# Optimization experiments

Hardware: AMD Instinct MI355X
Metric: run time of the kernel (lower is better)

The kernel has to match this reference:

```python
import jax, jax.numpy as jnp
import numpy as np

N = 50000      # nodes
E = 800000     # edges (avg degree 16)
F_IN = 64      # node_features (== GENConv out, so no input projection)
H = 64         # hidden
EXP = 2 * H    # GENConv MLP expansion dim = 128
D2 = F_IN + H  # dense-block concat dim = SAGEConv in = 128
EPS_MSG = 1e-7 # GENConv message eps
BN_EPS = 1e-5


def setup_inputs() -> dict:
    key = jax.random.key(0)
    ks = jax.random.split(key, 16)
    g = lambda k, shape, fan: jax.random.normal(k, shape, jnp.float32) / np.sqrt(fan)
    return {
        "x": jax.random.normal(ks[0], (N, F_IN), jnp.float32),
        "edge_index": jax.random.randint(ks[1], (2, E), 0, N, jnp.int32),
        # GENConv MLP: Linear(64,128) -> BatchNorm(128) -> ReLU -> Linear(128,64)
        "W1": g(ks[2], (H, EXP), H), "b1": jnp.zeros((EXP,), jnp.float32),
        "gamma": jnp.ones((EXP,), jnp.float32), "beta": jnp.zeros((EXP,), jnp.float32),
        "W2": g(ks[3], (EXP, H), EXP), "b2": jnp.zeros((H,), jnp.float32),
        # SAGEConv project Linear(128,128), lin_l Linear(128,64), lin_r Linear(128,64,bias=False)
        "Wp": g(ks[4], (D2, D2), D2), "bp": jnp.zeros((D2,), jnp.float32),
        "Wl": g(ks[5], (D2, H), D2), "bl": jnp.zeros((H,), jnp.float32),
        "Wr": g(ks[6], (D2, H), D2),
        # fc Linear(64,1)
        "Wf": g(ks[7], (H, 1), H), "bf": jnp.zeros((1,), jnp.float32),
    }


def _forward(x, W1, b1, gamma, beta, W2, b2, Wp, bp, Wl, bl, Wr, Wf, bf, src, dst):
    n = x.shape[0]
    # ---- GENConv(aggr='softmax', t=1.0): msg = relu(x_j) + eps -------------
    msg = jax.nn.relu(x[src]) + EPS_MSG                       # [E, H]
    mmax = jax.ops.segment_max(msg, dst, num_segments=n)      # per-dst, per-feature max
    mmax = jax.lax.stop_gradient(jnp.where(jnp.isfinite(mmax), mmax, 0.0))
    e = jnp.exp(msg - mmax[dst])                              # t = 1.0
    denom = jax.ops.segment_sum(e, dst, num_segments=n)
    numer = jax.ops.segment_sum(e * msg, dst, num_segments=n)
    agg = numer / jnp.where(denom > 0, denom, 1.0)            # softmax aggregation
    out = agg + x                                             # residual with x_dst
    # GENConv MLP (BatchNorm in training mode: batch stats, biased var)
    h = out @ W1 + b1
    mu = h.mean(axis=0)
    var = h.var(axis=0)
    h = (h - mu) * jax.lax.rsqrt(var + BN_EPS) * gamma + beta
    h = jax.nn.relu(h) @ W2 + b2                              # [N, H]
    # ---- DeepGCNLayer block='dense': concat input ---------------------------
    x2 = jnp.concatenate([x, h], axis=-1)                     # [N, F_IN+H]
    x2 = jax.nn.sigmoid(x2)                                   # self.relu = Sigmoid()
    # ---- SAGEConv(project=True, aggr=DeepSetsAggregation()==sum) -----------
    xp = jax.nn.relu(x2 @ Wp + bp)                            # projected source feats
    aggr = jax.ops.segment_sum(xp[src], dst, num_segments=n)  # DeepSets w/o nns = sum
    out2 = aggr @ Wl + bl + x2 @ Wr                           # root uses UNprojected x2
    out2 = jax.nn.sigmoid(out2)
    logits = out2 @ Wf + bf                                   # [N, 1]
    probs = jax.nn.sigmoid(logits)                            # training branch
    return probs, logits


def reference(x, edge_index, W1, b1, gamma, beta, W2, b2, Wp, bp, Wl, bl, Wr, Wf, bf):
    src, dst = edge_index[0], edge_index[1]
    return _forward(x, W1, b1, gamma, beta, W2, b2, Wp, bp, Wl, bl, Wr, Wf, bf, src, dst)
```

## Files before the change

### kernel.cpp

```cpp
#include <hip/hip_runtime.h>

#define F_IN 64
#define HID 64
#define EXPD 128
#define D2 128
#define MAXDEG 64
#define NPART 8

typedef __attribute__((ext_vector_type(8))) short bf16x8;
typedef __attribute__((ext_vector_type(4))) float f32x4;

__device__ __forceinline__ float sigmoidf_(float x) {
    return 1.0f / (1.0f + __expf(-x));
}
__device__ __forceinline__ unsigned bf16rne_(float f) {
    unsigned u = __float_as_uint(f);
    return (u + 0x7FFFu + ((u >> 16) & 1u)) >> 16;
}
__device__ __forceinline__ float bf16tof_(unsigned u16) {
    return __uint_as_float(u16 << 16);
}

__global__ __launch_bounds__(256) void k_prep(int* __restrict__ counts,
                                              float* __restrict__ bnsums,
                                              const float* __restrict__ x,
                                              unsigned short* __restrict__ x16,
                                              const float* __restrict__ W1,
                                              const float* __restrict__ W2,
                                              const float* __restrict__ Wp,
                                              const float* __restrict__ Wl,
                                              const float* __restrict__ Wr,
                                              short* __restrict__ dst, int n) {
    int b = blockIdx.x;
    int nzero = (n + 255) >> 8;
    if (b < nzero) {
        int i = b * 256 + threadIdx.x;
        if (i < n) counts[i] = 0;
        if (b == 0) bnsums[threadIdx.x] = 0.f;
        return;
    }
    if (b < nzero + 192) {
        int e = (b - nzero) * 256 + threadIdx.x;
        const float* src;
        int K, N, base;
        if (e < 8192)       { src = W1; K = 64;  N = 128; base = 0; }
        else if (e < 16384) { src = W2; K = 128; N = 64;  base = 8192; }
        else if (e < 32768) { src = Wp; K = 128; N = 128; base = 16384; }
        else if (e < 40960) { src = Wl; K = 128; N = 64;  base = 32768; }
        else                { src = Wr; K = 128; N = 64;  base = 40960; }
        int le = e - base;
        int j = le & 7;
        int lane = (le >> 3) & 63;
        int n16 = lane & 15, q = lane >> 4;
        int rest = le >> 9;
        int KC = K / 32;
        int kc = rest % KC, nt = rest / KC;
        int k = kc * 32 + q * 8 + j;
        int col = nt * 16 + n16;
        dst[e] = (short)bf16rne_(src[(size_t)k * N + col]);
        return;
    }
    int i0 = (b - nzero - 192) * 1024 + threadIdx.x * 4;
    if (i0 < n * F_IN) {
        float4 v = *(const float4*)(x + i0);
        uint2 pk;
        pk.x = bf16rne_(v.x) | (bf16rne_(v.y) << 16);
        pk.y = bf16rne_(v.z) | (bf16rne_(v.w) << 16);
        *(uint2*)(x16 + i0) = pk;
    }
}

__global__ __launch_bounds__(256) void k_fill(const int* __restrict__ ei,
                                              int* __restrict__ counts,
                                              unsigned short* __restrict__ csr,
                                              int nE, int n) {
    int p = blockIdx.x & (NPART - 1);
    int e = (blockIdx.x >> 3) * 256 + threadIdx.x;
    if (e >= nE) return;
    int d = ei[nE + e];
    int psz = (n + NPART - 1) / NPART;
    int lo = p * psz;
    if (d < lo || d >= lo + psz) return;
    int s = ei[e];
    int slot = atomicAdd(&counts[d], 1);
    if (slot < MAXDEG) csr[(size_t)d * MAXDEG + slot] = (unsigned short)s;
}

__global__ __launch_bounds__(256) void k_gen(const float* __restrict__ x,
                                             const unsigned short* __restrict__ x16,
                                             const int* __restrict__ counts,
                                             const unsigned short* __restrict__ csr,
                                             unsigned short* __restrict__ gen16, int n) {
    const unsigned* x32 = (const unsigned*)x16;
    int wid = threadIdx.x >> 6;
    int lane = threadIdx.x & 63;
    int H = lane >> 5, f2 = lane & 31;
    int v = blockIdx.x * 4 + wid;
    if (v >= n) return;
    int deg = counts[v];
    deg = deg > MAXDEG ? MAXDEG : deg;
    int idx = 0;
    if (lane < deg) idx = (int)csr[(size_t)v * MAXDEG + lane];
    float d0 = 0.f, d1 = 0.f, n0 = 0.f, n1 = 0.f;
    int i = 0;
    for (; i + 8 <= deg; i += 8) {
        int sA = __shfl(idx, i + 0 + H, 64);
        int sB = __shfl(idx, i + 2 + H, 64);
        int sC = __shfl(idx, i + 4 + H, 64);
        int sD = __shfl(idx, i + 6 + H, 64);
        unsigned uA = x32[(size_t)sA * 32 + f2];
        unsigned uB = x32[(size_t)sB * 32 + f2];
        unsigned uC = x32[(size_t)sC * 32 + f2];
        unsigned uD = x32[(size_t)sD * 32 + f2];
#pragma unroll
        for (int t = 0; t < 4; ++t) {
            unsigned u = t == 0 ? uA : t == 1 ? uB : t == 2 ? uC : uD;
            float m0 = fmaxf(bf16tof_(u & 0xFFFF), 0.f) + 1e-7f;
            float m1 = fmaxf(bf16tof_(u >> 16), 0.f) + 1e-7f;
            float e0 = __expf(m0), e1 = __expf(m1);
            d0 += e0; d1 += e1;
            n0 = fmaf(e0, m0, n0);
            n1 = fmaf(e1, m1, n1);
        }
    }
    for (; i + 2 <= deg; i += 2) {
        int s = __shfl(idx, i + H, 64);
        unsigned u = x32[(size_t)s * 32 + f2];
        float m0 = fmaxf(bf16tof_(u & 0xFFFF), 0.f) + 1e-7f;
        float m1 = fmaxf(bf16tof_(u >> 16), 0.f) + 1e-7f;
        float e0 = __expf(m0), e1 = __expf(m1);
        d0 += e0; d1 += e1;
        n0 = fmaf(e0, m0, n0);
        n1 = fmaf(e1, m1, n1);
    }
    if (i < deg) {
        int s = __shfl(idx, i, 64);
        if (H == 0) {
            unsigned u = x32[(size_t)s * 32 + f2];
            float m0 = fmaxf(bf16tof_(u & 0xFFFF), 0.f) + 1e-7f;
            float m1 = fmaxf(bf16tof_(u >> 16), 0.f) + 1e-7f;
            float e0 = __expf(m0), e1 = __expf(m1);
            d0 += e0; d1 += e1;
            n0 = fmaf(e0, m0, n0);
            n1 = fmaf(e1, m1, n1);
        }
    }
    d0 += __shfl_xor(d0, 32, 64);
    d1 += __shfl_xor(d1, 32, 64);
    n0 += __shfl_xor(n0, 32, 64);
    n1 += __shfl_xor(n1, 32, 64);
    if (H == 0) {
        float a0 = (deg > 0) ? (n0 / d0) : 0.f;
        float a1 = (deg > 0) ? (n1 / d1) : 0.f;
        float2 xv = *(const float2*)(x + (size_t)v * F_IN + f2 * 2);
        ((unsigned*)gen16)[(size_t)v * 32 + f2] =
            bf16rne_(a0 + xv.x) | (bf16rne_(a1 + xv.y) << 16);
    }
}

__global__ __launch_bounds__(256) void k_gemm1(const unsigned short* __restrict__ gen16,
                                               const short* __restrict__ Wf,
                                               const float* __restrict__ b1,
                                               unsigned short* __restrict__ h16,
                                               float* __restrict__ bnsums, int n) {
    __shared__ short As[64 * 64];
    __shared__ float bnred[256];
    int tid = threadIdx.x;
    int rblk = blockIdx.x * 64;
    if (tid < 256) bnred[tid] = 0.f;
#pragma unroll
    for (int it = 0; it < 2; ++it) {
        int c = it * 256 + tid;
        int rr = c & 63, q8 = c >> 6;
        int gr = rblk + rr;
        gr = gr < n ? gr : n - 1;
        uint4 v = *(const uint4*)(gen16 + (size_t)gr * F_IN + q8 * 8);
        int slot = ((rr >> 4) * 2 + (q8 >> 2)) * 64 + (q8 & 3) * 16 + (rr & 15);
        *(uint4*)(As + slot * 8) = v;
    }
    __syncthreads();
    int L = tid & 63, w = tid >> 6;
    int q = L >> 4, n16 = L & 15;
    int mt_base = (w & 1) * 2;
    int nt_base = (w >> 1) * 4;
    f32x4 acc[2][4];
#pragma unroll
    for (int mt = 0; mt < 2; ++mt)
#pragma unroll
        for (int nt = 0; nt < 4; ++nt) acc[mt][nt] = (f32x4){0.f, 0.f, 0.f, 0.f};
#pragma unroll
    for (int kc = 0; kc < 2; ++kc) {
        bf16x8 a0 = *(const bf16x8*)(As + (((mt_base + 0) * 2 + kc) * 64 + L) * 8);
        bf16x8 a1 = *(const bf16x8*)(As + (((mt_base + 1) * 2 + kc) * 64 + L) * 8);
#pragma unroll
        for (int nt = 0; nt < 4; ++nt) {
            bf16x8 b = *(const bf16x8*)(Wf + (size_t)(((nt_base + nt) * 2 + kc) * 64 + L) * 8);
            acc[0][nt] = __builtin_amdgcn_mfma_f32_16x16x32_bf16(a0, b, acc[0][nt], 0, 0, 0);
            acc[1][nt] = __builtin_amdgcn_mfma_f32_16x16x32_bf16(a1, b, acc[1][nt], 0, 0, 0);
        }
    }
#pragma unroll
    for (int nt = 0; nt < 4; ++nt) {
        int col = (nt_base + nt) * 16 + n16;
        float bv = b1[col];
        float s = 0.f, s2 = 0.f;
#pragma unroll
        for (int mt = 0; mt < 2; ++mt)
#pragma unroll
            for (int r = 0; r < 4; ++r) {
                int row = rblk + (w & 1) * 32 + mt * 16 + q * 4 + r;
                float hv = acc[mt][nt][r] + bv;
                if (row < n) {
                    h16[(size_t)row * EXPD + col] = (unsigned short)bf16rne_(hv);
                    s += hv;
                    s2 = fmaf(hv, hv, s2);
                }
            }
        s += __shfl_xor(s, 16, 64);
        s += __shfl_xor(s, 32, 64);
        s2 += __shfl_xor(s2, 16, 64);
        s2 += __shfl_xor(s2, 32, 64);
        if (q == 0) {
            atomicAdd(&bnred[col], s);
            atomicAdd(&bnred[128 + col], s2);
        }
    }
    __syncthreads();
    if (tid < 256) atomicAdd(&bnsums[tid], bnred[tid]);
}

__global__ __launch_bounds__(256) void k_mlp2a(const unsigned short* __restrict__ h16,
                                               const float* __restrict__ bnsums,
                                               const float* __restrict__ gamma,
                                               const float* __restrict__ beta,
                                               const short* __restrict__ Wf,
                                               const float* __restrict__ b2,
                                               const float* __restrict__ x,
                                               unsigned short* __restrict__ x2_16,
                                               float inv_n, int n) {
    __shared__ short As[128 * 128];
    __shared__ float ssl[256];
    int tid = threadIdx.x;
    int rblk = blockIdx.x * 128;
    if (tid < 128) {
        float mu = bnsums[tid] * inv_n;
        float var = fmaf(-mu, mu, bnsums[128 + tid] * inv_n);
        float rs = rsqrtf(fmaxf(var, 0.f) + 1e-5f);
        float scale = gamma[tid] * rs;
        ssl[tid] = scale;
        ssl[128 + tid] = fmaf(-mu, scale, beta[tid]);
    }
    __syncthreads();
#pragma unroll
    for (int it = 0; it < 8; ++it) {
        int c = it * 256 + tid;
        int rr = c & 127, q8 = c >> 7;
        int gr = rblk + rr;
        gr = gr < n ? gr : n - 1;
        uint4 v = *(const uint4*)(h16 + (size_t)gr * EXPD + q8 * 8);
        float4 sc1 = *(const float4*)(ssl + q8 * 8);
        float4 sc2 = *(const float4*)(ssl + q8 * 8 + 4);
        float4 sh1 = *(const float4*)(ssl + 128 + q8 * 8);
        float4 sh2 = *(const float4*)(ssl + 128 + q8 * 8 + 4);
        float o0 = fmaxf(fmaf(bf16tof_(v.x & 0xFFFF), sc1.x, sh1.x), 0.f);
        float o1 = fmaxf(fmaf(bf16tof_(v.x >> 16),    sc1.y, sh1.y), 0.f);
        float o2 = fmaxf(fmaf(bf16tof_(v.y & 0xFFFF), sc1.z, sh1.z), 0.f);
        float o3 = fmaxf(fmaf(bf16tof_(v.y >> 16),    sc1.w, sh1.w), 0.f);
        float o4 = fmaxf(fmaf(bf16tof_(v.z & 0xFFFF), sc2.x, sh2.x), 0.f);
        float o5 = fmaxf(fmaf(bf16tof_(v.z >> 16),    sc2.y, sh2.y), 0.f);
        float o6 = fmaxf(fmaf(bf16tof_(v.w & 0xFFFF), sc2.z, sh2.z), 0.f);
        float o7 = fmaxf(fmaf(bf16tof_(v.w >> 16),    sc2.w, sh2.w), 0.f);
        uint4 pk;
        pk.x = bf16rne_(o0) | (bf16rne_(o1) << 16);
        pk.y = bf16rne_(o2) | (bf16rne_(o3) << 16);
        pk.z = bf16rne_(o4) | (bf16rne_(o5) << 16);
        pk.w = bf16rne_(o6) | (bf16rne_(o7) << 16);
        int slot = ((rr >> 4) * 4 + (q8 >> 2)) * 64 + (q8 & 3) * 16 + (rr & 15);
        *(uint4*)(As + slot * 8) = pk;
    }
    __syncthreads();
    int L = tid & 63, w = tid >> 6;
    int q = L >> 4, n16 = L & 15;
    int mt_base = w * 2;
    f32x4 acc[2][4];
#pragma unroll
    for (int mt = 0; mt < 2; ++mt)
#pragma unroll
        for (int nt = 0; nt < 4; ++nt) acc[mt][nt] = (f32x4){0.f, 0.f, 0.f, 0.f};
#pragma unroll
    for (int kc = 0; kc < 4; ++kc) {
        bf16x8 a0 = *(const bf16x8*)(As + (((mt_base + 0) * 4 + kc) * 64 + L) * 8);
        bf16x8 a1 = *(const bf16x8*)(As + (((mt_base + 1) * 4 + kc) * 64 + L) * 8);
#pragma unroll
        for (int nt = 0; nt < 4; ++nt) {
            bf16x8 b = *(const bf16x8*)(Wf + (size_t)((nt * 4 + kc) * 64 + L) * 8);
            acc[0][nt] = __builtin_amdgcn_mfma_f32_16x16x32_bf16(a0, b, acc[0][nt], 0, 0, 0);
            acc[1][nt] = __builtin_amdgcn_mfma_f32_16x16x32_bf16(a1, b, acc[1][nt], 0, 0, 0);
        }
    }
#pragma unroll
    for (int it = 0; it < 8; ++it) {
        int i = it * 256 + tid;
        int rr = i >> 4, c4 = i & 15;
        int row = rblk + rr;
        if (row < n) {
            float4 xv = *(const float4*)(x + (size_t)row * F_IN + c4 * 4);
            uint2 pk;
            pk.x = bf16rne_(sigmoidf_(xv.x)) | (bf16rne_(sigmoidf_(xv.y)) << 16);
            pk.y = bf16rne_(sigmoidf_(xv.z)) | (bf16rne_(sigmoidf_(xv.w)) << 16);
            *(uint2*)(x2_16 + (size_t)row * D2 + c4 * 4) = pk;
        }
    }
#pragma unroll
    for (int nt = 0; nt < 4; ++nt) {
        int col = nt * 16 + n16;
        float bv = b2[col];
#pragma unroll
        for (int mt = 0; mt < 2; ++mt)
#pragma unroll
            for (int r = 0; r < 4; ++r) {
                int row = rblk + w * 32 + mt * 16 + q * 4 + r;
                if (row < n)
                    x2_16[(size_t)row * D2 + 64 + col] =
                        (unsigned short)bf16rne_(sigmoidf_(acc[mt][nt][r] + bv));
            }
    }
}

__global__ __launch_bounds__(256) void k_mlp2b(const unsigned short* __restrict__ x2_16,
                                               const short* __restrict__ Wfp,
                                               const short* __restrict__ Wfl,
                                               const float* __restrict__ bp,
                                               unsigned short* __restrict__ yp16, int n) {
    __shared__ short As[64 * 128];
    int tid = threadIdx.x;
    int rblk = blockIdx.x * 64;
#pragma unroll
    for (int it = 0; it < 4; ++it) {
        int c = it * 256 + tid;
        int rr = c & 63, q8 = c >> 6;
        int gr = rblk + rr;
        gr = gr < n ? gr : n - 1;
        uint4 v = *(const uint4*)(x2_16 + (size_t)gr * D2 + q8 * 8);
        int slot = ((rr >> 4) * 4 + (q8 >> 2)) * 64 + (q8 & 3) * 16 + (rr & 15);
        *(uint4*)(As + slot * 8) = v;
    }
    __syncthreads();
    int L = tid & 63, w = tid >> 6;
    int q = L >> 4, n16 = L & 15;
    int mt_base = (w & 1) * 2;
    int nt_base = (w >> 1) * 4;
    f32x4 acc[2][4];
#pragma unroll
    for (int mt = 0; mt < 2; ++mt)
#pragma unroll
        for (int nt = 0; nt < 4; ++nt) acc[mt][nt] = (f32x4){0.f, 0.f, 0.f, 0.f};
#pragma unroll
    for (int kc = 0; kc < 4; ++kc) {
        bf16x8 a0 = *(const bf16x8*)(As + (((mt_base + 0) * 4 + kc) * 64 + L) * 8);
        bf16x8 a1 = *(const bf16x8*)(As + (((mt_base + 1) * 4 + kc) * 64 + L) * 8);
#pragma unroll
        for (int nt = 0; nt < 4; ++nt) {
            bf16x8 b = *(const bf16x8*)(Wfp + (size_t)(((nt_base + nt) * 4 + kc) * 64 + L) * 8);
            acc[0][nt] = __builtin_amdgcn_mfma_f32_16x16x32_bf16(a0, b, acc[0][nt], 0, 0, 0);
            acc[1][nt] = __builtin_amdgcn_mfma_f32_16x16x32_bf16(a1, b, acc[1][nt], 0, 0, 0);
        }
    }
    __syncthreads();
#pragma unroll
    for (int nt = 0; nt < 4; ++nt) {
        int kk = (nt_base + nt) * 16 + n16;
        float bv = bp[kk];
        int q8b = kk >> 3, jb = kk & 7;
#pragma unroll
        for (int mt = 0; mt < 2; ++mt)
#pragma unroll
            for (int r = 0; r < 4; ++r) {
                int rr2 = (w & 1) * 32 + mt * 16 + q * 4 + r;
                float xv = fmaxf(acc[mt][nt][r] + bv, 0.f);
                int slot = ((rr2 >> 4) * 4 + (q8b >> 2)) * 64 + (q8b & 3) * 16 + (rr2 & 15);
                As[slot * 8 + jb] = (short)bf16rne_(xv);
            }
    }
    __syncthreads();
    f32x4 acc2[4];
#pragma unroll
    for (int nt = 0; nt < 4; ++nt) acc2[nt] = (f32x4){0.f, 0.f, 0.f, 0.f};
#pragma unroll
    for (int kc = 0; kc < 4; ++kc) {
        bf16x8 a = *(const bf16x8*)(As + ((w * 4 + kc) * 64 + L) * 8);
#pragma unroll
        for (int nt = 0; nt < 4; ++nt) {
            bf16x8 b = *(const bf16x8*)(Wfl + (size_t)((nt * 4 + kc) * 64 + L) * 8);
            acc2[nt] = __builtin_amdgcn_mfma_f32_16x16x32_bf16(a, b, acc2[nt], 0, 0, 0);
        }
    }
#pragma unroll
    for (int nt = 0; nt < 4; ++nt) {
        int col = nt * 16 + n16;
#pragma unroll
        for (int r = 0; r < 4; ++r) {
            int row = rblk + w * 16 + q * 4 + r;
            if (row < n)
                yp16[(size_t)row * HID + col] = (unsigned short)bf16rne_(acc2[nt][r]);
        }
    }
}

__global__ __launch_bounds__(256) void k_sage(const unsigned short* __restrict__ yp16,
                                              const int* __restrict__ counts,
                                              const unsigned short* __restrict__ csr,
                                              unsigned short* __restrict__ aggr16, int n) {
    const unsigned* yp32 = (const unsigned*)yp16;
    int wid = threadIdx.x >> 6;
    int lane = threadIdx.x & 63;
    int H = lane >> 5, f2 = lane & 31;
    int v = blockIdx.x * 4 + wid;
    if (v >= n) return;
    int deg = counts[v];
    deg = deg > MAXDEG ? MAXDEG : deg;
    int idx = 0;
    if (lane < deg) idx = (int)csr[(size_t)v * MAXDEG + lane];
    float a0 = 0.f, a1 = 0.f;
    int i = 0;
    for (; i + 8 <= deg; i += 8) {
        int sA = __shfl(idx, i + 0 + H, 64);
        int sB = __shfl(idx, i + 2 + H, 64);
        int sC = __shfl(idx, i + 4 + H, 64);
        int sD = __shfl(idx, i + 6 + H, 64);
        unsigned uA = yp32[(size_t)sA * 32 + f2];
        unsigned uB = yp32[(size_t)sB * 32 + f2];
        unsigned uC = yp32[(size_t)sC * 32 + f2];
        unsigned uD = yp32[(size_t)sD * 32 + f2];
        a0 += bf16tof_(uA & 0xFFFF) + bf16tof_(uB & 0xFFFF) +
              bf16tof_(uC & 0xFFFF) + bf16tof_(uD & 0xFFFF);
        a1 += bf16tof_(uA >> 16) + bf16tof_(uB >> 16) +
              bf16tof_(uC >> 16) + bf16tof_(uD >> 16);
    }
    for (; i + 2 <= deg; i += 2) {
        int s = __shfl(idx, i + H, 64);
        unsigned u = yp32[(size_t)s * 32 + f2];
        a0 += bf16tof_(u & 0xFFFF);
        a1 += bf16tof_(u >> 16);
    }
    if (i < deg) {
        int s = __shfl(idx, i, 64);
        if (H == 0) {
            unsigned u = yp32[(size_t)s * 32 + f2];
            a0 += bf16tof_(u & 0xFFFF);
            a1 += bf16tof_(u >> 16);
        }
    }
    a0 += __shfl_xor(a0, 32, 64);
    a1 += __shfl_xor(a1, 32, 64);
    if (H == 0)
        ((unsigned*)aggr16)[(size_t)v * 32 + f2] = bf16rne_(a0) | (bf16rne_(a1) << 16);
}

__global__ __launch_bounds__(256) void k_final(const unsigned short* __restrict__ aggr16,
                                               const unsigned short* __restrict__ x2_16,
                                               const short* __restrict__ Wfr,
                                               const float* __restrict__ bl,
                                               const float* __restrict__ Wfv,
                                               const float* __restrict__ bf,
                                               float* __restrict__ out, int n) {
    __shared__ short As[128 * 128];
    int tid = threadIdx.x;
    int rblk = blockIdx.x * 128;
#pragma unroll
    for (int it = 0; it < 8; ++it) {
        int c = it * 256 + tid;
        int rr = c & 127, q8 = c >> 7;
        int gr = rblk + rr;
        gr = gr < n ? gr : n - 1;
        uint4 v = *(const uint4*)(x2_16 + (size_t)gr * D2 + q8 * 8);
        int slot = ((rr >> 4) * 4 + (q8 >> 2)) * 64 + (q8 & 3) * 16 + (rr & 15);
        *(uint4*)(As + slot * 8) = v;
    }
    __syncthreads();
    int L = tid & 63, w = tid >> 6;
    int q = L >> 4, n16 = L & 15;
    int mt_base = w * 2;
    f32x4 acc[2][4];
#pragma unroll
    for (int mt = 0; mt < 2; ++mt)
#pragma unroll
        for (int nt = 0; nt < 4; ++nt) acc[mt][nt] = (f32x4){0.f, 0.f, 0.f, 0.f};
#pragma unroll
    for (int kc = 0; kc < 4; ++kc) {
        bf16x8 a0 = *(const bf16x8*)(As + (((mt_base + 0) * 4 + kc) * 64 + L) * 8);
        bf16x8 a1 = *(const bf16x8*)(As + (((mt_base + 1) * 4 + kc) * 64 + L) * 8);
#pragma unroll
        for (int nt = 0; nt < 4; ++nt) {
            bf16x8 b = *(const bf16x8*)(Wfr + (size_t)((nt * 4 + kc) * 64 + L) * 8);
            acc[0][nt] = __builtin_amdgcn_mfma_f32_16x16x32_bf16(a0, b, acc[0][nt], 0, 0, 0);
            acc[1][nt] = __builtin_amdgcn_mfma_f32_16x16x32_bf16(a1, b, acc[1][nt], 0, 0, 0);
        }
    }
    float blv[4], wfv[4];
#pragma unroll
    for (int nt = 0; nt < 4; ++nt) {
        blv[nt] = bl[nt * 16 + n16];
        wfv[nt] = Wfv[nt * 16 + n16];
    }
    float bf0 = bf[0];
#pragma unroll
    for (int mt = 0; mt < 2; ++mt)
#pragma unroll
        for (int r = 0; r < 4; ++r) {
            int row = rblk + w * 32 + mt * 16 + q * 4 + r;
            int rowc = row < n ? row : n - 1;
            float t = 0.f;
#pragma unroll
            for (int nt = 0; nt < 4; ++nt) {
                float ag = bf16tof_(aggr16[(size_t)rowc * HID + nt * 16 + n16]);
                t = fmaf(sigmoidf_(acc[mt][nt][r] + blv[nt] + ag), wfv[nt], t);
            }
            t += __shfl_xor(t, 1, 64);
            t += __shfl_xor(t, 2, 64);
            t += __shfl_xor(t, 4, 64);
            t += __shfl_xor(t, 8, 64);
            if (n16 == 0 && row < n) {
                float lg = t + bf0;
                out[row] = sigmoidf_(lg);
                out[n + row] = lg;
            }
        }
}

extern "C" void kernel_launch(void* const* d_in, const int* in_sizes, int n_in,
                              void* d_out, int out_size, void* d_ws, size_t ws_size,
                              hipStream_t stream) {
    const float* x     = (const float*)d_in[0];
    const int*   ei    = (const int*)d_in[1];
    const float* W1    = (const float*)d_in[2];
    const float* b1    = (const float*)d_in[3];
    const float* gamma = (const float*)d_in[4];
    const float* beta  = (const float*)d_in[5];
    const float* W2    = (const float*)d_in[6];
    const float* b2    = (const float*)d_in[7];
    const float* Wp    = (const float*)d_in[8];
    const float* bp    = (const float*)d_in[9];
    const float* Wl    = (const float*)d_in[10];
    const float* bl    = (const float*)d_in[11];
    const float* Wr    = (const float*)d_in[12];
    const float* Wfv   = (const float*)d_in[13];
    const float* bf    = (const float*)d_in[14];
    const int n = in_sizes[0] / F_IN;
    const int e = in_sizes[1] / 2;

    char* ws = (char*)d_ws;
    size_t off = 0;
    auto alloc = [&](size_t bytes) -> void* {
        void* p = (void*)(ws + off);
        off += (bytes + 255) & ~(size_t)255;
        return p;
    };
    int*            counts = (int*)alloc((size_t)n * 4);
    unsigned short* csr    = (unsigned short*)alloc((size_t)n * MAXDEG * 2);
    float*          bnsums = (float*)alloc(256 * 4);
    unsigned short* x16    = (unsigned short*)alloc((size_t)n * F_IN * 2);
    unsigned short* gen16  = (unsigned short*)alloc((size_t)n * F_IN * 2);
    unsigned short* h16    = (unsigned short*)alloc((size_t)n * EXPD * 2);
    unsigned short* x2_16  = (unsigned short*)alloc((size_t)n * D2 * 2);
    unsigned short* yp16   = (unsigned short*)alloc((size_t)n * HID * 2);
    unsigned short* aggr16 = (unsigned short*)alloc((size_t)n * HID * 2);
    short*          wfrag  = (short*)alloc(49152 * 2);

    float* out = (float*)d_out;
    const int nb64  = (n + 63) / 64;
    const int nb128 = (n + 127) / 128;
    const int nb4   = (n + 3) / 4;
    const int nprep = ((n + 255) / 256) + 192 + ((n * F_IN + 1023) / 1024);

    k_prep<<<nprep, 256, 0, stream>>>(counts, bnsums, x, x16, W1, W2, Wp, Wl, Wr,
                                      wfrag, n);
    k_fill<<<((e + 255) / 256) * NPART, 256, 0, stream>>>(ei, counts, csr, e, n);
    k_gen<<<nb4, 256, 0, stream>>>(x, x16, counts, csr, gen16, n);
    k_gemm1<<<nb64, 256, 0, stream>>>(gen16, wfrag, b1, h16, bnsums, n);
    k_mlp2a<<<nb128, 256, 0, stream>>>(h16, bnsums, gamma, beta, wfrag + 8192, b2,
                                       x, x2_16, 1.0f / (float)n, n);
    k_mlp2b<<<nb64, 256, 0, stream>>>(x2_16, wfrag + 16384, wfrag + 32768, bp,
                                      yp16, n);
    k_sage<<<nb4, 256, 0, stream>>>(yp16, counts, csr, aggr16, n);
    k_final<<<nb128, 256, 0, stream>>>(aggr16, x2_16, wfrag + 40960, bl, Wfv, bf,
                                       out, n);
}
```

Baseline: 242.9 us.

## Merge CSR fill with prep, memset counters, widen gathers to 4 features per lane

Replaces the zeroing part of the prep kernel with a hipMemsetAsync over counts and bnsums, then fuses the CSR fill into the weight and x conversion kernel, removing one launch. The GENConv and SAGE gather kernels now have each lane load 8 bytes (4 bf16 features) and handle 4 edges per wave step instead of 2, cutting shuffle and loop overhead. Residual and sigmoid reads of x use the bf16 copy instead of fp32, reducing bandwidth at some precision cost in the residual and concat inputs.

Result: no change. 245.3 us (+1.0%).

```diff
diff --git a/kernel.cpp b/kernel.cpp
--- a/kernel.cpp
+++ b/kernel.cpp
@@ -21,26 +21,35 @@
     return __uint_as_float(u16 << 16);
 }
 
-__global__ __launch_bounds__(256) void k_prep(int* __restrict__ counts,
-                                              float* __restrict__ bnsums,
-                                              const float* __restrict__ x,
-                                              unsigned short* __restrict__ x16,
-                                              const float* __restrict__ W1,
-                                              const float* __restrict__ W2,
-                                              const float* __restrict__ Wp,
-                                              const float* __restrict__ Wl,
-                                              const float* __restrict__ Wr,
-                                              short* __restrict__ dst, int n) {
+__global__ __launch_bounds__(256) void k_fillprep(const int* __restrict__ ei,
+                                                  int* __restrict__ counts,
+                                                  unsigned short* __restrict__ csr,
+                                                  const float* __restrict__ x,
+                                                  unsigned short* __restrict__ x16,
+                                                  const float* __restrict__ W1,
+                                                  const float* __restrict__ W2,
+                                                  const float* __restrict__ Wp,
+                                                  const float* __restrict__ Wl,
+                                                  const float* __restrict__ Wr,
+                                                  short* __restrict__ dst,
+                                                  int nE, int n, int nfillb) {
     int b = blockIdx.x;
-    int nzero = (n + 255) >> 8;
-    if (b < nzero) {
-        int i = b * 256 + threadIdx.x;
-        if (i < n) counts[i] = 0;
-        if (b == 0) bnsums[threadIdx.x] = 0.f;
+    if (b < nfillb) {
+        int p = b & (NPART - 1);
+        int e = (b >> 3) * 256 + threadIdx.x;
+        if (e >= nE) return;
+        int d = ei[nE + e];
+        int psz = (n + NPART - 1) / NPART;
+        int lo = p * psz;
+        if (d < lo || d >= lo + psz) return;
+        int s = ei[e];
+        int slot = atomicAdd(&counts[d], 1);
+        if (slot < MAXDEG) csr[(size_t)d * MAXDEG + slot] = (unsigned short)s;
         return;
     }
-    if (b < nzero + 192) {
-        int e = (b - nzero) * 256 + threadIdx.x;
+    b -= nfillb;
+    if (b < 192) {
+        int e = b * 256 + threadIdx.x;
         const float* src;
         int K, N, base;
         if (e < 8192)       { src = W1; K = 64;  N = 128; base = 0; }
@@ -60,7 +69,7 @@
         dst[e] = (short)bf16rne_(src[(size_t)k * N + col]);
         return;
     }
-    int i0 = (b - nzero - 192) * 1024 + threadIdx.x * 4;
+    int i0 = (b - 192) * 1024 + threadIdx.x * 4;
     if (i0 < n * F_IN) {
         float4 v = *(const float4*)(x + i0);
         uint2 pk;
@@ -70,91 +79,75 @@
     }
 }
 
-__global__ __launch_bounds__(256) void k_fill(const int* __restrict__ ei,
-                                              int* __restrict__ counts,
-                                              unsigned short* __restrict__ csr,
-                                              int nE, int n) {
-    int p = blockIdx.x & (NPART - 1);
-    int e = (blockIdx.x >> 3) * 256 + threadIdx.x;
-    if (e >= nE) return;
-    int d = ei[nE + e];
-    int psz = (n + NPART - 1) / NPART;
-    int lo = p * psz;
-    if (d < lo || d >= lo + psz) return;
-    int s = ei[e];
-    int slot = atomicAdd(&counts[d], 1);
-    if (slot < MAXDEG) csr[(size_t)d * MAXDEG + slot] = (unsigned short)s;
-}
-
-__global__ __launch_bounds__(256) void k_gen(const float* __restrict__ x,
-                                             const unsigned short* __restrict__ x16,
+__global__ __launch_bounds__(256) void k_gen(const unsigned short* __restrict__ x16,
                                              const int* __restrict__ counts,
                                              const unsigned short* __restrict__ csr,
                                              unsigned short* __restrict__ gen16, int n) {
-    const unsigned* x32 = (const unsigned*)x16;
+    const uint2* x64 = (const uint2*)x16;
     int wid = threadIdx.x >> 6;
     int lane = threadIdx.x & 63;
-    int H = lane >> 5, f2 = lane & 31;
+    int Q = lane >> 4, f4 = lane & 15;
     int v = blockIdx.x * 4 + wid;
     if (v >= n) return;
     int deg = counts[v];
     deg = deg > MAXDEG ? MAXDEG : deg;
     int idx = 0;
     if (lane < deg) idx = (int)csr[(size_t)v * MAXDEG + lane];
-    float d0 = 0.f, d1 = 0.f, n0 = 0.f, n1 = 0.f;
+    float d0 = 0.f, d1 = 0.f, d2 = 0.f, d3 = 0.f;
+    float n0 = 0.f, n1 = 0.f, n2 = 0.f, n3 = 0.f;
+#define GEN_PROC(u)                                                         \
+    {                                                                       \
+        float m0 = fmaxf(bf16tof_((u).x & 0xFFFF), 0.f) + 1e-7f;            \
+        float m1 = fmaxf(bf16tof_((u).x >> 16), 0.f) + 1e-7f;               \
+        float m2 = fmaxf(bf16tof_((u).y & 0xFFFF), 0.f) + 1e-7f;            \
+        float m3 = fmaxf(bf16tof_((u).y >> 16), 0.f) + 1e-7f;               \
+        float e0 = __expf(m0), e1 = __expf(m1), e2 = __expf(m2), e3 = __expf(m3); \
+        d0 += e0; d1 += e1; d2 += e2; d3 += e3;                             \
+        n0 = fmaf(e0, m0, n0); n1 = fmaf(e1, m1, n1);                       \
+        n2 = fmaf(e2, m2, n2); n3 = fmaf(e3, m3, n3);                       \
+    }
     int i = 0;
-    for (; i + 8 <= deg; i += 8) {
-        int sA = __shfl(idx, i + 0 + H, 64);
-        int sB = __shfl(idx, i + 2 + H, 64);
-        int sC = __shfl(idx, i + 4 + H, 64);
-        int sD = __shfl(idx, i + 6 + H, 64);
-        unsigned uA = x32[(size_t)sA * 32 + f2];
-        unsigned uB = x32[(size_t)sB * 32 + f2];
-        unsigned uC = x32[(size_t)sC * 32 + f2];
-        unsigned uD = x32[(size_t)sD * 32 + f2];
-#pragma unroll
-        for (int t = 0; t < 4; ++t) {
-            unsigned u = t == 0 ? uA : t == 1 ? uB : t == 2 ? uC : uD;
-            float m0 = fmaxf(bf16tof_(u & 0xFFFF), 0.f) + 1e-7f;
-            float m1 = fmaxf(bf16tof_(u >> 16), 0.f) + 1e-7f;
-            float e0 = __expf(m0), e1 = __expf(m1);
-            d0 += e0; d1 += e1;
-            n0 = fmaf(e0, m0, n0);
-            n1 = fmaf(e1, m1, n1);
-        }
-    }
-    for (; i + 2 <= deg; i += 2) {
-        int s = __shfl(idx, i + H, 64);
-        unsigned u = x32[(size_t)s * 32 + f2];
-        float m0 = fmaxf(bf16tof_(u & 0xFFFF), 0.f) + 1e-7f;
-        float m1 = fmaxf(bf16tof_(u >> 16), 0.f) + 1e-7f;
-        float e0 = __expf(m0), e1 = __expf(m1);
-        d0 += e0; d1 += e1;
-        n0 = fmaf(e0, m0, n0);
-        n1 = fmaf(e1, m1, n1);
-    }
-    if (i < deg) {
-        int s = __shfl(idx, i, 64);
-        if (H == 0) {
-            unsigned u = x32[(size_t)s * 32 + f2];
-            float m0 = fmaxf(bf16tof_(u & 0xFFFF), 0.f) + 1e-7f;
-            float m1 = fmaxf(bf16tof_(u >> 16), 0.f) + 1e-7f;
-            float e0 = __expf(m0), e1 = __expf(m1);
-            d0 += e0; d1 += e1;
-            n0 = fmaf(e0, m0, n0);
-            n1 = fmaf(e1, m1, n1);
-        }
-    }
-    d0 += __shfl_xor(d0, 32, 64);
-    d1 += __shfl_xor(d1, 32, 64);
-    n0 += __shfl_xor(n0, 32, 64);
-    n1 += __shfl_xor(n1, 32, 64);
-    if (H == 0) {
+    for (; i + 16 <= deg; i += 16) {
+        int sA = __shfl(idx, i + Q, 64);
+        int sB = __shfl(idx, i + 4 + Q, 64);
+        int sC = __shfl(idx, i + 8 + Q, 64);
+        int sD = __shfl(idx, i + 12 + Q, 64);
+        uint2 uA = x64[(size_t)sA * 16 + f4];
+        uint2 uB = x64[(size_t)sB * 16 + f4];
+        uint2 uC = x64[(size_t)sC * 16 + f4];
+        uint2 uD = x64[(size_t)sD * 16 + f4];
+        GEN_PROC(uA); GEN_PROC(uB); GEN_PROC(uC); GEN_PROC(uD);
+    }
+    for (; i < deg; i += 4) {
+        int s = __shfl(idx, i + Q, 64);
+        if (Q < deg - i) {
+            uint2 u = x64[(size_t)s * 16 + f4];
+            GEN_PROC(u);
+        }
+    }
+#undef GEN_PROC
+    d0 += __shfl_xor(d0, 16, 64); d0 += __shfl_xor(d0, 32, 64);
+    d1 += __shfl_xor(d1, 16, 64); d1 += __shfl_xor(d1, 32, 64);
+    d2 += __shfl_xor(d2, 16, 64); d2 += __shfl_xor(d2, 32, 64);
+    d3 += __shfl_xor(d3, 16, 64); d3 += __shfl_xor(d3, 32, 64);
+    n0 += __shfl_xor(n0, 16, 64); n0 += __shfl_xor(n0, 32, 64);
+    n1 += __shfl_xor(n1, 16, 64); n1 += __shfl_xor(n1, 32, 64);
+    n2 += __shfl_xor(n2, 16, 64); n2 += __shfl_xor(n2, 32, 64);
+    n3 += __shfl_xor(n3, 16, 64); n3 += __shfl_xor(n3, 32, 64);
+    if (Q == 0) {
         float a0 = (deg > 0) ? (n0 / d0) : 0.f;
         float a1 = (deg > 0) ? (n1 / d1) : 0.f;
-        float2 xv = *(const float2*)(x + (size_t)v * F_IN + f2 * 2);
-        ((unsigned*)gen16)[(size_t)v * 32 + f2] =
-            bf16rne_(a0 + xv.x) | (bf16rne_(a1 + xv.y) << 16);
+        float a2 = (deg > 0) ? (n2 / d2) : 0.f;
+        float a3 = (deg > 0) ? (n3 / d3) : 0.f;
+        uint2 xv = x64[(size_t)v * 16 + f4];
+        float r0 = a0 + bf16tof_(xv.x & 0xFFFF);
+        float r1 = a1 + bf16tof_(xv.x >> 16);
+        float r2 = a2 + bf16tof_(xv.y & 0xFFFF);
+        float r3 = a3 + bf16tof_(xv.y >> 16);
+        uint2 o;
+        o.x = bf16rne_(r0) | (bf16rne_(r1) << 16);
+        o.y = bf16rne_(r2) | (bf16rne_(r3) << 16);
+        ((uint2*)gen16)[(size_t)v * 16 + f4] = o;
     }
 }
 
@@ -235,7 +228,7 @@
                                                const float* __restrict__ beta,
                                                const short* __restrict__ Wf,
                                                const float* __restrict__ b2,
-                                               const float* __restrict__ x,
+                                               const unsigned short* __restrict__ x16,
                                                unsigned short* __restrict__ x2_16,
                                                float inv_n, int n) {
     __shared__ short As[128 * 128];
@@ -304,10 +297,14 @@
         int rr = i >> 4, c4 = i & 15;
         int row = rblk + rr;
         if (row < n) {
-            float4 xv = *(const float4*)(x + (size_t)row * F_IN + c4 * 4);
+            uint2 xv = ((const uint2*)x16)[(size_t)row * 16 + c4];
+            float s0 = sigmoidf_(bf16tof_(xv.x & 0xFFFF));
+            float s1 = sigmoidf_(bf16tof_(xv.x >> 16));
+            float s2 = sigmoidf_(bf16tof_(xv.y & 0xFFFF));
+            float s3 = sigmoidf_(bf16tof_(xv.y >> 16));
             uint2 pk;
-            pk.x = bf16rne_(sigmoidf_(xv.x)) | (bf16rne_(sigmoidf_(xv.y)) << 16);
-            pk.y = bf16rne_(sigmoidf_(xv.z)) | (bf16rne_(sigmoidf_(xv.w)) << 16);
+            pk.x = bf16rne_(s0) | (bf16rne_(s1) << 16);
+            pk.y = bf16rne_(s2) | (bf16rne_(s3) << 16);
             *(uint2*)(x2_16 + (size_t)row * D2 + c4 * 4) = pk;
         }
     }
@@ -411,50 +408,54 @@
                                               const int* __restrict__ counts,
                                               const unsigned short* __restrict__ csr,
                                               unsigned short* __restrict__ aggr16, int n) {
-    const unsigned* yp32 = (const unsigned*)yp16;
+    const uint2* yp64 = (const uint2*)yp16;
     int wid = threadIdx.x >> 6;
     int lane = threadIdx.x & 63;
-    int H = lane >> 5, f2 = lane & 31;
+    int Q = lane >> 4, f4 = lane & 15;
     int v = blockIdx.x * 4 + wid;
     if (v >= n) return;
     int deg = counts[v];
     deg = deg > MAXDEG ? MAXDEG : deg;
     int idx = 0;
     if (lane < deg) idx = (int)csr[(size_t)v * MAXDEG + lane];
-    float a0 = 0.f, a1 = 0.f;
+    float a0 = 0.f, a1 = 0.f, a2 = 0.f, a3 = 0.f;
+#define SAGE_PROC(u)                                \
+    {                                               \
+        a0 += bf16tof_((u).x & 0xFFFF);             \
+        a1 += bf16tof_((u).x >> 16);                \
+        a2 += bf16tof_((u).y & 0xFFFF);             \
+        a3 += bf16tof_((u).y >> 16);                \
+    }
     int i = 0;
-    for (; i + 8 <= deg; i += 8) {
-        int sA = __shfl(idx, i + 0 + H, 64);
-        int sB = __shfl(idx, i + 2 + H, 64);
-        int sC = __shfl(idx, i + 4 + H, 64);
-        int sD = __shfl(idx, i + 6 + H, 64);
-        unsigned uA = yp32[(size_t)sA * 32 + f2];
-        unsigned uB = yp32[(size_t)sB * 32 + f2];
-        unsigned uC = yp32[(size_t)sC * 32 + f2];
-        unsigned uD = yp32[(size_t)sD * 32 + f2];
-        a0 += bf16tof_(uA & 0xFFFF) + bf16tof_(uB & 0xFFFF) +
-              bf16tof_(uC & 0xFFFF) + bf16tof_(uD & 0xFFFF);
-        a1 += bf16tof_(uA >> 16) + bf16tof_(uB >> 16) +
-              bf16tof_(uC >> 16) + bf16tof_(uD >> 16);
-    }
-    for (; i + 2 <= deg; i += 2) {
-        int s = __shfl(idx, i + H, 64);
-        unsigned u = yp32[(size_t)s * 32 + f2];
-        a0 += bf16tof_(u & 0xFFFF);
-        a1 += bf16tof_(u >> 16);
-    }
-    if (i < deg) {
-        int s = __shfl(idx, i, 64);
-        if (H == 0) {
-            unsigned u = yp32[(size_t)s * 32 + f2];
-            a0 += bf16tof_(u & 0xFFFF);
-            a1 += bf16tof_(u >> 16);
-        }
-    }
-    a0 += __shfl_xor(a0, 32, 64);
-    a1 += __shfl_xor(a1, 32, 64);
-    if (H == 0)
-        ((unsigned*)aggr16)[(size_t)v * 32 + f2] = bf16rne_(a0) | (bf16rne_(a1) << 16);
+    for (; i + 16 <= deg; i += 16) {
+        int sA = __shfl(idx, i + Q, 64);
+        int sB = __shfl(idx, i + 4 + Q, 64);
+        int sC = __shfl(idx, i + 8 + Q, 64);
+        int sD = __shfl(idx, i + 12 + Q, 64);
+        uint2 uA = yp64[(size_t)sA * 16 + f4];
+        uint2 uB = yp64[(size_t)sB * 16 + f4];
+        uint2 uC = yp64[(size_t)sC * 16 + f4];
+        uint2 uD = yp64[(size_t)sD * 16 + f4];
+        SAGE_PROC(uA); SAGE_PROC(uB); SAGE_PROC(uC); SAGE_PROC(uD);
+    }
+    for (; i < deg; i += 4) {
+        int s = __shfl(idx, i + Q, 64);
+        if (Q < deg - i) {
+            uint2 u = yp64[(size_t)s * 16 + f4];
+            SAGE_PROC(u);
+        }
+    }
+#undef SAGE_PROC
+    a0 += __shfl_xor(a0, 16, 64); a0 += __shfl_xor(a0, 32, 64);
+    a1 += __shfl_xor(a1, 16, 64); a1 += __shfl_xor(a1, 32, 64);
+    a2 += __shfl_xor(a2, 16, 64); a2 += __shfl_xor(a2, 32, 64);
+    a3 += __shfl_xor(a3, 16, 64); a3 += __shfl_xor(a3, 32, 64);
+    if (Q == 0) {
+        uint2 o;
+        o.x = bf16rne_(a0) | (bf16rne_(a1) << 16);
+        o.y = bf16rne_(a2) | (bf16rne_(a3) << 16);
+        ((uint2*)aggr16)[(size_t)v * 16 + f4] = o;
+    }
 }
 
 __global__ __launch_bounds__(256) void k_final(const unsigned short* __restrict__ aggr16,
@@ -557,8 +558,8 @@
         return p;
     };
     int*            counts = (int*)alloc((size_t)n * 4);
+    float*          bnsums = (float*)alloc(256 * 4);
     unsigned short* csr    = (unsigned short*)alloc((size_t)n * MAXDEG * 2);
-    float*          bnsums = (float*)alloc(256 * 4);
     unsigned short* x16    = (unsigned short*)alloc((size_t)n * F_IN * 2);
     unsigned short* gen16  = (unsigned short*)alloc((size_t)n * F_IN * 2);
     unsigned short* h16    = (unsigned short*)alloc((size_t)n * EXPD * 2);
@@ -571,15 +572,18 @@
     const int nb64  = (n + 63) / 64;
     const int nb128 = (n + 127) / 128;
     const int nb4   = (n + 3) / 4;
-    const int nprep = ((n + 255) / 256) + 192 + ((n * F_IN + 1023) / 1024);
-
-    k_prep<<<nprep, 256, 0, stream>>>(counts, bnsums, x, x16, W1, W2, Wp, Wl, Wr,
-                                      wfrag, n);
-    k_fill<<<((e + 255) / 256) * NPART, 256, 0, stream>>>(ei, counts, csr, e, n);
-    k_gen<<<nb4, 256, 0, stream>>>(x, x16, counts, csr, gen16, n);
+    const int nfillb = ((e + 255) / 256) * NPART;
+    const int nfp = nfillb + 192 + ((n * F_IN + 1023) / 1024);
+
+    size_t zlen = ((((size_t)n * 4) + 255) & ~(size_t)255) + 1024;
+    hipMemsetAsync(counts, 0, zlen, stream);
+
+    k_fillprep<<<nfp, 256, 0, stream>>>(ei, counts, csr, x, x16, W1, W2, Wp, Wl,
+                                        Wr, wfrag, e, n, nfillb);
+    k_gen<<<nb4, 256, 0, stream>>>(x16, counts, csr, gen16, n);
     k_gemm1<<<nb64, 256, 0, stream>>>(gen16, wfrag, b1, h16, bnsums, n);
     k_mlp2a<<<nb128, 256, 0, stream>>>(h16, bnsums, gamma, beta, wfrag + 8192, b2,
-                                       x, x2_16, 1.0f / (float)n, n);
+                                       x16, x2_16, 1.0f / (float)n, n);
     k_mlp2b<<<nb64, 256, 0, stream>>>(x2_16, wfrag + 16384, wfrag + 32768, bp,
                                       yp16, n);
     k_sage<<<nb4, 256, 0, stream>>>(yp16, counts, csr, aggr16, n);
```

## Fuse CSR fill into prep kernel, memset counters, read bf16 x downstream

Applied to the files above, without the earlier changes.

Zeroing of the degree counters and BN sums moves to a single hipMemsetAsync, and the CSR edge fill is merged into the prep kernel, dropping the 8-way partitioned fill pass that reread the edge list once per partition. The GEN residual and the sigmoid(x) half of x2 now read the bf16 copy of x instead of the fp32 original, halving those reads. The trade-off is that atomics are no longer grouped by destination partition, which may hurt locality. Using bf16 x in the residual and sigmoid also adds extra rounding error.

Measured after the change: 247.0 us. About the same (+1.7%).

```diff
diff --git a/kernel.cpp b/kernel.cpp
--- a/kernel.cpp
+++ b/kernel.cpp
@@ -5,7 +5,6 @@
 #define EXPD 128
 #define D2 128
 #define MAXDEG 64
-#define NPART 8
 
 typedef __attribute__((ext_vector_type(8))) short bf16x8;
 typedef __attribute__((ext_vector_type(4))) float f32x4;
@@ -21,26 +20,31 @@
     return __uint_as_float(u16 << 16);
 }
 
-__global__ __launch_bounds__(256) void k_prep(int* __restrict__ counts,
-                                              float* __restrict__ bnsums,
-                                              const float* __restrict__ x,
-                                              unsigned short* __restrict__ x16,
-                                              const float* __restrict__ W1,
-                                              const float* __restrict__ W2,
-                                              const float* __restrict__ Wp,
-                                              const float* __restrict__ Wl,
-                                              const float* __restrict__ Wr,
-                                              short* __restrict__ dst, int n) {
+__global__ __launch_bounds__(256) void k_fillprep(const int* __restrict__ ei,
+                                                  int* __restrict__ counts,
+                                                  unsigned short* __restrict__ csr,
+                                                  const float* __restrict__ x,
+                                                  unsigned short* __restrict__ x16,
+                                                  const float* __restrict__ W1,
+                                                  const float* __restrict__ W2,
+                                                  const float* __restrict__ Wp,
+                                                  const float* __restrict__ Wl,
+                                                  const float* __restrict__ Wr,
+                                                  short* __restrict__ dst,
+                                                  int nE, int n, int nfillb) {
     int b = blockIdx.x;
-    int nzero = (n + 255) >> 8;
-    if (b < nzero) {
-        int i = b * 256 + threadIdx.x;
-        if (i < n) counts[i] = 0;
-        if (b == 0) bnsums[threadIdx.x] = 0.f;
+    if (b < nfillb) {
+        int e = b * 256 + threadIdx.x;
+        if (e >= nE) return;
+        int s = ei[e];
+        int d = ei[nE + e];
+        int slot = atomicAdd(&counts[d], 1);
+        if (slot < MAXDEG) csr[(size_t)d * MAXDEG + slot] = (unsigned short)s;
         return;
     }
-    if (b < nzero + 192) {
-        int e = (b - nzero) * 256 + threadIdx.x;
+    b -= nfillb;
+    if (b < 192) {
+        int e = b * 256 + threadIdx.x;
         const float* src;
         int K, N, base;
         if (e < 8192)       { src = W1; K = 64;  N = 128; base = 0; }
@@ -60,7 +64,7 @@
         dst[e] = (short)bf16rne_(src[(size_t)k * N + col]);
         return;
     }
-    int i0 = (b - nzero - 192) * 1024 + threadIdx.x * 4;
+    int i0 = (b - 192) * 1024 + threadIdx.x * 4;
     if (i0 < n * F_IN) {
         float4 v = *(const float4*)(x + i0);
         uint2 pk;
@@ -70,24 +74,7 @@
     }
 }
 
-__global__ __launch_bounds__(256) void k_fill(const int* __restrict__ ei,
-                                              int* __restrict__ counts,
-                                              unsigned short* __restrict__ csr,
-                                              int nE, int n) {
-    int p = blockIdx.x & (NPART - 1);
-    int e = (blockIdx.x >> 3) * 256 + threadIdx.x;
-    if (e >= nE) return;
-    int d = ei[nE + e];
-    int psz = (n + NPART - 1) / NPART;
-    int lo = p * psz;
-    if (d < lo || d >= lo + psz) return;
-    int s = ei[e];
-    int slot = atomicAdd(&counts[d], 1);
-    if (slot < MAXDEG) csr[(size_t)d * MAXDEG + slot] = (unsigned short)s;
-}
-
-__global__ __launch_bounds__(256) void k_gen(const float* __restrict__ x,
-                                             const unsigned short* __restrict__ x16,
+__global__ __launch_bounds__(256) void k_gen(const unsigned short* __restrict__ x16,
                                              const int* __restrict__ counts,
                                              const unsigned short* __restrict__ csr,
                                              unsigned short* __restrict__ gen16, int n) {
@@ -152,9 +139,11 @@
     if (H == 0) {
         float a0 = (deg > 0) ? (n0 / d0) : 0.f;
         float a1 = (deg > 0) ? (n1 / d1) : 0.f;
-        float2 xv = *(const float2*)(x + (size_t)v * F_IN + f2 * 2);
+        unsigned xv = x32[(size_t)v * 32 + f2];
+        float r0 = a0 + bf16tof_(xv & 0xFFFF);
+        float r1 = a1 + bf16tof_(xv >> 16);
         ((unsigned*)gen16)[(size_t)v * 32 + f2] =
-            bf16rne_(a0 + xv.x) | (bf16rne_(a1 + xv.y) << 16);
+            bf16rne_(r0) | (bf16rne_(r1) << 16);
     }
 }
 
@@ -235,7 +224,7 @@
                                                const float* __restrict__ beta,
                                                const short* __restrict__ Wf,
                                                const float* __restrict__ b2,
-                                               const float* __restrict__ x,
+                                               const unsigned short* __restrict__ x16,
                                                unsigned short* __restrict__ x2_16,
                                                float inv_n, int n) {
     __shared__ short As[128 * 128];
@@ -304,10 +293,14 @@
         int rr = i >> 4, c4 = i & 15;
         int row = rblk + rr;
         if (row < n) {
-            float4 xv = *(const float4*)(x + (size_t)row * F_IN + c4 * 4);
+            uint2 xv = ((const uint2*)x16)[(size_t)row * 16 + c4];
+            float s0 = sigmoidf_(bf16tof_(xv.x & 0xFFFF));
+            float s1 = sigmoidf_(bf16tof_(xv.x >> 16));
+            float s2 = sigmoidf_(bf16tof_(xv.y & 0xFFFF));
+            float s3 = sigmoidf_(bf16tof_(xv.y >> 16));
             uint2 pk;
-            pk.x = bf16rne_(sigmoidf_(xv.x)) | (bf16rne_(sigmoidf_(xv.y)) << 16);
-            pk.y = bf16rne_(sigmoidf_(xv.z)) | (bf16rne_(sigmoidf_(xv.w)) << 16);
+            pk.x = bf16rne_(s0) | (bf16rne_(s1) << 16);
+            pk.y = bf16rne_(s2) | (bf16rne_(s3) << 16);
             *(uint2*)(x2_16 + (size_t)row * D2 + c4 * 4) = pk;
         }
     }
@@ -557,8 +550,8 @@
         return p;
     };
     int*            counts = (int*)alloc((size_t)n * 4);
+    float*          bnsums = (float*)alloc(256 * 4);
     unsigned short* csr    = (unsigned short*)alloc((size_t)n * MAXDEG * 2);
-    float*          bnsums = (float*)alloc(256 * 4);
     unsigned short* x16    = (unsigned short*)alloc((size_t)n * F_IN * 2);
     unsigned short* gen16  = (unsigned short*)alloc((size_t)n * F_IN * 2);
     unsigned short* h16    = (unsigned short*)alloc((size_t)n * EXPD * 2);
@@ -571,15 +564,18 @@
     const int nb64  = (n + 63) / 64;
     const int nb128 = (n + 127) / 128;
     const int nb4   = (n + 3) / 4;
-    const int nprep = ((n + 255) / 256) + 192 + ((n * F_IN + 1023) / 1024);
-
-    k_prep<<<nprep, 256, 0, stream>>>(counts, bnsums, x, x16, W1, W2, Wp, Wl, Wr,
-                                      wfrag, n);
-    k_fill<<<((e + 255) / 256) * NPART, 256, 0, stream>>>(ei, counts, csr, e, n);
-    k_gen<<<nb4, 256, 0, stream>>>(x, x16, counts, csr, gen16, n);
+    const int nfillb = (e + 255) / 256;
+    const int nfp = nfillb + 192 + ((n * F_IN + 1023) / 1024);
+
+    size_t zlen = ((((size_t)n * 4) + 255) & ~(size_t)255) + 1024;
+    hipMemsetAsync(counts, 0, zlen, stream);
+
+    k_fillprep<<<nfp, 256, 0, stream>>>(ei, counts, csr, x, x16, W1, W2, Wp, Wl,
+                                        Wr, wfrag, e, n, nfillb);
+    k_gen<<<nb4, 256, 0, stream>>>(x16, counts, csr, gen16, n);
     k_gemm1<<<nb64, 256, 0, stream>>>(gen16, wfrag, b1, h16, bnsums, n);
     k_mlp2a<<<nb128, 256, 0, stream>>>(h16, bnsums, gamma, beta, wfrag + 8192, b2,
-                                       x, x2_16, 1.0f / (float)n, n);
+                                       x16, x2_16, 1.0f / (float)n, n);
     k_mlp2b<<<nb64, 256, 0, stream>>>(x2_16, wfrag + 16384, wfrag + 32768, bp,
                                       yp16, n);
     k_sage<<<nb4, 256, 0, stream>>>(yp16, counts, csr, aggr16, n);
```
